# Performance work log

Measured on AMD Instinct MI355X. Metric: run time of the kernel, lower is better.

Reference implementation:

```python
import jax, jax.numpy as jnp
import numpy as np

B, N, IN_FEAT, HID, NHEAD, NLAYER, K = 8, 2048, 512, 128, 4, 3, 8
GRAPH_DIM = 32
EPS = 1e-5


def _layernorm(x, g, b):
    m = x.mean(-1, keepdims=True)
    v = ((x - m) ** 2).mean(-1, keepdims=True)
    return (x - m) * jax.lax.rsqrt(v + EPS) * g + b


def _knn_adj(cent):
    # cent [B,Ni,2] -> symmetric bool adjacency [B,Ni,Ni]; each node's k nearest
    # neighbours (self included, dist 0), then bidirected union (to_bidirected).
    d2 = jnp.sum((cent[:, :, None, :] - cent[:, None, :, :]) ** 2, -1)
    _, idx = jax.lax.top_k(-d2, K)  # [B,Ni,K]
    Bc, Nc = cent.shape[0], cent.shape[1]
    mask = jnp.zeros((Bc, Nc, Nc), bool).at[
        jnp.arange(Bc)[:, None, None], jnp.arange(Nc)[None, :, None], idx].set(True)
    return mask | jnp.swapaxes(mask, 1, 2)


def setup_inputs():
    key = jax.random.key(0)
    ks = jax.random.split(key, 12)
    s = 0.05
    H = HID
    return dict(
        feats=jax.random.normal(ks[0], (B, N, IN_FEAT), jnp.float32),
        cent=jax.random.uniform(ks[1], (B, N, 2), jnp.float32),
        Wp1=jax.random.normal(ks[2], (IN_FEAT, H)) * s, bp1=jnp.zeros((H,)),
        bn_g=jnp.ones((H,)), bn_b=jnp.zeros((H,)),
        Wp2=jax.random.normal(ks[3], (H, H)) * s, bp2=jnp.zeros((H,)),
        g1=jnp.ones((NLAYER, H)), be1=jnp.zeros((NLAYER, H)),
        g2=jnp.ones((NLAYER, H)), be2=jnp.zeros((NLAYER, H)),
        Ws=jax.random.normal(ks[4], (NLAYER, NHEAD, H, H)) * s,
        Wn=jax.random.normal(ks[5], (NLAYER, NHEAD, H, H)) * s,
        bs=jnp.zeros((NLAYER, NHEAD, H)),
        Wg=jax.random.normal(ks[6], (NLAYER, NHEAD * H, H)) * s,
        bg=jnp.zeros((NLAYER, H)),
        W1=jax.random.normal(ks[7], (NLAYER, H, H)) * s, b1=jnp.zeros((NLAYER, H)),
        W2=jax.random.normal(ks[8], (NLAYER, H, H)) * s, b2=jnp.zeros((NLAYER, H)),
        Wq=jax.random.normal(ks[9], (NLAYER, H, 1)) * s, bq=jnp.zeros((NLAYER,)),
        Wf1=jax.random.normal(ks[10], (2 * H, H)) * s, bf1=jnp.zeros((H,)),
        Wf2=jax.random.normal(ks[11], (H, GRAPH_DIM)) * s, bf2=jnp.zeros((GRAPH_DIM,)),
    )


def reference(feats, cent, Wp1, bp1, bn_g, bn_b, Wp2, bp2,
              g1, be1, g2, be2, Ws, Wn, bs, Wg, bg,
              W1, b1, W2, b2, Wq, bq, Wf1, bf1, Wf2, bf2):
    # preconv: Linear -> BatchNorm1d(eval: running mean 0 / var 1) -> ReLU -> Linear
    x = feats @ Wp1 + bp1
    x = x * (bn_g / jnp.sqrt(1.0 + EPS)) + bn_b
    x = jax.nn.relu(x) @ Wp2 + bp2              # [B,N,H]
    c = cent
    picks = 0.0
    for i in range(NLAYER):
        A = _knn_adj(c).astype(x.dtype)          # dynamic KNN graph, [B,Ni,Ni]
        deg = A.sum(-1)                          # in-degree (>=1, self loop)
        # GraphTransformerLayer: pre-LN -> multi-head mean SAGEConv -> residual
        xn = _layernorm(x, g1[i], be1[i])
        m = jnp.einsum('bij,bjd->bid', A, xn) / deg[..., None]
        h = jnp.einsum('bnd,hde->bnhe', xn, Ws[i]) \
            + jnp.einsum('bnd,hde->bnhe', m, Wn[i]) + bs[i]
        Bc, Nc = h.shape[0], h.shape[1]
        h = h.reshape(Bc, Nc, NHEAD * HID)       # concat heads on feature dim
        x = x + jax.nn.relu(h) @ Wg[i] + bg[i]
        # FFN block with residual
        xn2 = _layernorm(x, g2[i], be2[i])
        x = x + jax.nn.relu(xn2 @ W1[i] + b1[i]) @ W2[i] + b2[i]
        # SAGPool: GraphConv (symmetric norm) score -> top-k ratio 0.5 -> gate
        dinv = jax.lax.rsqrt(deg)
        s = dinv * jnp.einsum('bij,bj->bi', A, dinv * (x @ Wq[i])[..., 0]) + bq[i]
        kkeep = Nc // 2
        topv, topi = jax.lax.top_k(s, kkeep)     # per-graph top nodes
        x = jnp.take_along_axis(x, topi[..., None], axis=1) * jnp.tanh(topv)[..., None]
        c = jnp.take_along_axis(c, topi[..., None], axis=1)
        # max + avg readout on pooled graph
        picks = picks + jnp.concatenate([x.max(axis=1), x.mean(axis=1)], axis=-1)
    f = jax.nn.relu(picks @ Wf1 + bf1)
    f = jax.nn.relu(f @ Wf2 + bf2)               # [B, GRAPH_DIM]
    return f
```

## Files before the change

### kernel.cpp

```cpp
#include <hip/hip_runtime.h>
#include <math.h>

#define EPSV 1e-5f
#define GF_RELU 1
#define GF_ACCUM 2

typedef unsigned long long u64;
typedef unsigned int u32;
typedef unsigned short u16;
typedef float v2f __attribute__((ext_vector_type(2)));
typedef short bf16x8 __attribute__((ext_vector_type(8)));
typedef float f32x4 __attribute__((ext_vector_type(4)));

static const int Bn = 8;
static const int Nmax = 2048;
static const int KNN_K = 8;

__device__ __forceinline__ u32 split_pack(float v) {
  u32 u = __float_as_uint(v);
  float r = v - __uint_as_float(u & 0xffff0000u);
  return (u >> 16) | (__float_as_uint(r) & 0xffff0000u);
}

__device__ __forceinline__ void split4(float4 v, uint2& hp, uint2& lp) {
// ... 182 lines not shown
                                                        const float* __restrict__ be,
                                                        float* __restrict__ xn) {
  int row = blockIdx.x * 4 + (threadIdx.x >> 6);
  int lane = threadIdx.x & 63;
  const float* xr = x + (size_t)row * 128;
  float v1 = xr[lane], v2 = xr[lane + 64];
  float s = v1 + v2;
  for (int off = 32; off >= 1; off >>= 1) s += __shfl_xor(s, off, 64);
  float mean = s / 128.0f;
  float d1 = v1 - mean, d2 = v2 - mean;
  float q = d1 * d1 + d2 * d2;
  for (int off = 32; off >= 1; off >>= 1) q += __shfl_xor(q, off, 64);
  float rs = rsqrtf(q / 128.0f + EPSV);
  float* xo = xn + (size_t)row * 128;
  xo[lane] = d1 * rs * g[lane] + be[lane];
  xo[lane + 64] = d2 * rs * g[lane + 64] + be[lane + 64];
}

__global__ __launch_bounds__(256) void aggregate_kernel(const u32* __restrict__ adj,
                                                        const float* __restrict__ xn,
                                                        float* __restrict__ m,
                                                        float* __restrict__ dinv, int Ni) {
  int sub = threadIdx.x >> 7;
  int t = threadIdx.x & 127;
  int i = blockIdx.x * 2 + sub, b = blockIdx.y;
  __shared__ int cnt[2];
  extern __shared__ int list[];
  int* lst = list + sub * Ni;
  if (t == 0) cnt[sub] = 0;
  __syncthreads();
  int wpr = Ni >> 5;
  for (int w = t; w < wpr; w += 128) {
    u32 bits = adj[((size_t)(b * Nmax + i)) * 64 + w];
    while (bits) {
      int bit = __ffs(bits) - 1;
      bits &= bits - 1;
      int pos = atomicAdd(&cnt[sub], 1);
      lst[pos] = (w << 5) + bit;
    }
  }
  __syncthreads();
  int d = cnt[sub];
  float a0 = 0.0f, a1 = 0.0f;
  int k = 0;
  for (; k + 2 <= d; k += 2) {
    a0 += xn[((size_t)b * Ni + lst[k]) * 128 + t];
    a1 += xn[((size_t)b * Ni + lst[k + 1]) * 128 + t];
  }
  if (k < d) a0 += xn[((size_t)b * Ni + lst[k]) * 128 + t];
  m[((size_t)b * Ni + i) * 128 + t] = (a0 + a1) / (float)d;
  if (t == 0) dinv[b * Nmax + i] = 1.0f / sqrtf((float)d);
}

__global__ __launch_bounds__(256) void attn_gemm1_kernel(
    const float* __restrict__ XN, const float* __restrict__ MM,
    const u32* __restrict__ Wc, const float* __restrict__ bs,
    u16* __restrict__ Hh, u16* __restrict__ Hl, int M) {
  __shared__ u16 Ah[128][40], Al[128][40], Bh[128][40], Bl[128][40];
  int tid = threadIdx.x;
  int lane = tid & 63, w = tid >> 6;
  int wr = w >> 1, wc = w & 1;
  int lr = lane & 15, lk = (lane >> 4) * 8;
  int rowBase = blockIdx.y * 128, colBase = blockIdx.x * 128;
  f32x4 acc[4][4] = {};
  int arow = tid >> 1, aq = (tid & 1) * 16;
  int bcol = tid >> 1, bq = (tid & 1) * 16;

  float4 af[4];
  uint4 bf[4];
  {
    const float* Ap = XN + (size_t)(rowBase + arow) * 128 + aq;
#pragma unroll
    for (int q = 0; q < 4; ++q) af[q] = *(const float4*)(Ap + 4 * q);
    const u32* Bp = Wc + (size_t)(colBase + bcol) * 256 + bq;
#pragma unroll
    for (int q = 0; q < 4; ++q) bf[q] = *(const uint4*)(Bp + 4 * q);
  }
  for (int t = 0; t < 8; ++t) {
    __syncthreads();
#pragma unroll
    for (int q = 0; q < 4; ++q) {
      uint2 hp, lp;
      split4(af[q], hp, lp);
      *(uint2*)&Ah[arow][aq + 4 * q] = hp;
      *(uint2*)&Al[arow][aq + 4 * q] = lp;
      depair4(bf[q], hp, lp);
      *(uint2*)&Bh[bcol][bq + 4 * q] = hp;
      *(uint2*)&Bl[bcol][bq + 4 * q] = lp;
    }
    __syncthreads();
    if (t + 1 < 8) {
      const float* Asrc = (t + 1 < 4) ? XN : MM;
      int k0 = ((t + 1) & 3) * 32;
      const float* Ap = Asrc + (size_t)(rowBase + arow) * 128 + k0 + aq;
#pragma unroll
      for (int q = 0; q < 4; ++q) af[q] = *(const float4*)(Ap + 4 * q);
      const u32* Bp = Wc + (size_t)(colBase + bcol) * 256 + (t + 1) * 32 + bq;
#pragma unroll
      for (int q = 0; q < 4; ++q) bf[q] = *(const uint4*)(Bp + 4 * q);
    }
    bf16x8 ah[4], al[4], bh[4], bl[4];
#pragma unroll
    for (int mi = 0; mi < 4; ++mi) {
      int ar = wr * 64 + mi * 16 + lr;
      ah[mi] = *(const bf16x8*)&Ah[ar][lk];
      al[mi] = *(const bf16x8*)&Al[ar][lk];
    }
#pragma unroll
    for (int ni = 0; ni < 4; ++ni) {
      int bc = wc * 64 + ni * 16 + lr;
      bh[ni] = *(const bf16x8*)&Bh[bc][lk];
      bl[ni] = *(const bf16x8*)&Bl[bc][lk];
    }
#pragma unroll
    for (int mi = 0; mi < 4; ++mi)
#pragma unroll
      for (int ni = 0; ni < 4; ++ni) {
        f32x4 c = acc[mi][ni];
        c = __builtin_amdgcn_mfma_f32_16x16x32_bf16(al[mi], bh[ni], c, 0, 0, 0);
        c = __builtin_amdgcn_mfma_f32_16x16x32_bf16(ah[mi], bl[ni], c, 0, 0, 0);
        c = __builtin_amdgcn_mfma_f32_16x16x32_bf16(ah[mi], bh[ni], c, 0, 0, 0);
        acc[mi][ni] = c;
      }
  }
  int rq = (lane >> 4) * 4;
#pragma unroll
  for (int ni = 0; ni < 4; ++ni) {
    int col = colBase + wc * 64 + ni * 16 + lr;
    float bv = bs[col];
    size_t cbase = (size_t)(col >> 3) * 128 + (col & 7);
#pragma unroll
    for (int mi = 0; mi < 4; ++mi) {
      int rb = (rowBase >> 4) + wr * 4 + mi;
#pragma unroll
      for (int r = 0; r < 4; ++r) {
        float v = fmaxf(acc[mi][ni][r] + bv, 0.0f);
        u32 pr = split_pack(v);
        size_t o = (size_t)rb * 8192 + cbase + (size_t)(rq + r) * 8;
        Hh[o] = (u16)pr;
        Hl[o] = (u16)(pr >> 16);
      }
    }
  }
}

__global__ __launch_bounds__(256) void attn2_ffn16_kernel(
    const u16* __restrict__ Hh, const u16* __restrict__ Hl,
    const u16* __restrict__ Bgh, const u16* __restrict__ Bgl,
    const float* __restrict__ bg, const float* __restrict__ g,
    const float* __restrict__ be,
    const u16* __restrict__ W1h, const u16* __restrict__ W1l,
    const float* __restrict__ b1,
    const u16* __restrict__ W2h, const u16* __restrict__ W2l,
    const float* __restrict__ b2, float* __restrict__ x, int M) {
  __shared__ float XF[16][132];
  __shared__ u16 XH[16][136], XL[16][136];
  int tid = threadIdx.x;
  int lane = tid & 63, w = tid >> 6;
  int lr = lane & 15, lk = (lane >> 4) * 8, rq = (lane >> 4) * 4;
  int rowBase = blockIdx.x * 16;
  int colW = w * 32;
  int fo = (lane >> 4) * 128 + lr * 8;

  f32x4 acc[2] = {};
  {
    const u16* pAh = Hh + (size_t)blockIdx.x * 8192;
    const u16* pAl = Hl + (size_t)blockIdx.x * 8192;
    const u16* pBh = Bgh + (size_t)(w * 2) * 8192;
    const u16* pBl = Bgl + (size_t)(w * 2) * 8192;
    bf16x8 ah = *(const bf16x8*)(pAh + fo);
    bf16x8 al = *(const bf16x8*)(pAl + fo);
    bf16x8 b0h = *(const bf16x8*)(pBh + fo);
    bf16x8 b0l = *(const bf16x8*)(pBl + fo);
    bf16x8 b1h = *(const bf16x8*)(pBh + 8192 + fo);
    bf16x8 b1l = *(const bf16x8*)(pBl + 8192 + fo);
    for (int kt = 0; kt < 16; ++kt) {
      bf16x8 cah = ah, cal = al, cb0h = b0h, cb0l = b0l, cb1h = b1h, cb1l = b1l;
      if (kt + 1 < 16) {
        int off = (kt + 1) * 512 + fo;
        ah = *(const bf16x8*)(pAh + off);
        al = *(const bf16x8*)(pAl + off);
        b0h = *(const bf16x8*)(pBh + off);
        b0l = *(const bf16x8*)(pBl + off);
        b1h = *(const bf16x8*)(pBh + 8192 + off);
        b1l = *(const bf16x8*)(pBl + 8192 + off);
      }
      acc[0] = __builtin_amdgcn_mfma_f32_16x16x32_bf16(cal, cb0h, acc[0], 0, 0, 0);
      acc[0] = __builtin_amdgcn_mfma_f32_16x16x32_bf16(cah, cb0l, acc[0], 0, 0, 0);
      acc[0] = __builtin_amdgcn_mfma_f32_16x16x32_bf16(cah, cb0h, acc[0], 0, 0, 0);
      acc[1] = __builtin_amdgcn_mfma_f32_16x16x32_bf16(cal, cb1h, acc[1], 0, 0, 0);
      acc[1] = __builtin_amdgcn_mfma_f32_16x16x32_bf16(cah, cb1l, acc[1], 0, 0, 0);
      acc[1] = __builtin_amdgcn_mfma_f32_16x16x32_bf16(cah, cb1h, acc[1], 0, 0, 0);
    }
  }
#pragma unroll
  for (int ni = 0; ni < 2; ++ni) {
    int col = colW + ni * 16 + lr;
    float bv = bg[col];
#pragma unroll
    for (int r = 0; r < 4; ++r) {
      int rowL = rq + r;
      size_t o = (size_t)(rowBase + rowL) * 128 + col;
      float v = x[o] + acc[ni][r] + bv;
      x[o] = v;
      XF[rowL][col] = v;
    }
  }
  __syncthreads();
#pragma unroll
  for (int rr = 0; rr < 4; ++rr) {
    int rowL = w * 4 + rr;
    float v1 = XF[rowL][lane], v2 = XF[rowL][64 + lane];
    float s = v1 + v2;
    for (int off = 32; off >= 1; off >>= 1) s += __shfl_xor(s, off, 64);
    float mean = s / 128.0f;
    float d1 = v1 - mean, d2 = v2 - mean;
    float q = d1 * d1 + d2 * d2;
    for (int off = 32; off >= 1; off >>= 1) q += __shfl_xor(q, off, 64);
    float rs = rsqrtf(q / 128.0f + EPSV);
    float xn1 = d1 * rs * g[lane] + be[lane];
    float xn2 = d2 * rs * g[lane + 64] + be[lane + 64];
    u32 p1 = split_pack(xn1);
    u32 p2 = split_pack(xn2);
    XH[rowL][lane] = (u16)p1;  XL[rowL][lane] = (u16)(p1 >> 16);
    XH[rowL][64 + lane] = (u16)p2;  XL[rowL][64 + lane] = (u16)(p2 >> 16);
  }
  __syncthreads();
  f32x4 acc1[2] = {};
  {
    const u16* pBh = W1h + (size_t)(w * 2) * 2048;
    const u16* pBl = W1l + (size_t)(w * 2) * 2048;
#pragma unroll
    for (int kt = 0; kt < 4; ++kt) {
      int k0 = kt * 32 + lk;
      int off = kt * 512 + fo;
      bf16x8 ah = *(const bf16x8*)&XH[lr][k0];
      bf16x8 al = *(const bf16x8*)&XL[lr][k0];
      bf16x8 b0h = *(const bf16x8*)(pBh + off);
      bf16x8 b0l = *(const bf16x8*)(pBl + off);
      bf16x8 b1h = *(const bf16x8*)(pBh + 2048 + off);
      bf16x8 b1l = *(const bf16x8*)(pBl + 2048 + off);
      acc1[0] = __builtin_amdgcn_mfma_f32_16x16x32_bf16(al, b0h, acc1[0], 0, 0, 0);
      acc1[0] = __builtin_amdgcn_mfma_f32_16x16x32_bf16(ah, b0l, acc1[0], 0, 0, 0);
      acc1[0] = __builtin_amdgcn_mfma_f32_16x16x32_bf16(ah, b0h, acc1[0], 0, 0, 0);
      acc1[1] = __builtin_amdgcn_mfma_f32_16x16x32_bf16(al, b1h, acc1[1], 0, 0, 0);
      acc1[1] = __builtin_amdgcn_mfma_f32_16x16x32_bf16(ah, b1l, acc1[1], 0, 0, 0);
      acc1[1] = __builtin_amdgcn_mfma_f32_16x16x32_bf16(ah, b1h, acc1[1], 0, 0, 0);
    }
  }
  __syncthreads();
#pragma unroll
  for (int ni = 0; ni < 2; ++ni) {
    int col = colW + ni * 16 + lr;
    float bv = b1[col];
#pragma unroll
    for (int r = 0; r < 4; ++r) {
      int rowL = rq + r;
      float v = fmaxf(acc1[ni][r] + bv, 0.0f);
      u32 pr = split_pack(v);
      XH[rowL][col] = (u16)pr;
      XL[rowL][col] = (u16)(pr >> 16);
    }
  }
  __syncthreads();
  f32x4 acc2[2] = {};
  {
    const u16* pBh = W2h + (size_t)(w * 2) * 2048;
    const u16* pBl = W2l + (size_t)(w * 2) * 2048;
#pragma unroll
    for (int kt = 0; kt < 4; ++kt) {
      int k0 = kt * 32 + lk;
      int off = kt * 512 + fo;
      bf16x8 ah = *(const bf16x8*)&XH[lr][k0];
      bf16x8 al = *(const bf16x8*)&XL[lr][k0];
      bf16x8 b0h = *(const bf16x8*)(pBh + off);
      bf16x8 b0l = *(const bf16x8*)(pBl + off);
      bf16x8 b1h = *(const bf16x8*)(pBh + 2048 + off);
      bf16x8 b1l = *(const bf16x8*)(pBl + 2048 + off);
      acc2[0] = __builtin_amdgcn_mfma_f32_16x16x32_bf16(al, b0h, acc2[0], 0, 0, 0);
      acc2[0] = __builtin_amdgcn_mfma_f32_16x16x32_bf16(ah, b0l, acc2[0], 0, 0, 0);
      acc2[0] = __builtin_amdgcn_mfma_f32_16x16x32_bf16(ah, b0h, acc2[0], 0, 0, 0);
      acc2[1] = __builtin_amdgcn_mfma_f32_16x16x32_bf16(al, b1h, acc2[1], 0, 0, 0);
      acc2[1] = __builtin_amdgcn_mfma_f32_16x16x32_bf16(ah, b1l, acc2[1], 0, 0, 0);
      acc2[1] = __builtin_amdgcn_mfma_f32_16x16x32_bf16(ah, b1h, acc2[1], 0, 0, 0);
    }
  }
#pragma unroll
  for (int ni = 0; ni < 2; ++ni) {
    int col = colW + ni * 16 + lr;
    float bv = b2[col];
#pragma unroll
    for (int r = 0; r < 4; ++r) {
      int rowL = rq + r;
      size_t o = (size_t)(rowBase + rowL) * 128 + col;
      x[o] += acc2[ni][r] + bv;
    }
  }
}

__global__ __launch_bounds__(256) void preconv1_kernel(
    const float* __restrict__ F, const u32* __restrict__ WT,
    const float* __restrict__ sc, const float* __restrict__ bb,
    u32* __restrict__ H, int M) {
  __shared__ u16 Ah[64][40], Al[64][40], Bh[128][40], Bl[128][40];
  int tid = threadIdx.x;
  int lane = tid & 63, w = tid >> 6;
  int wr = w >> 1, wc = w & 1;
  int lr = lane & 15, lk = (lane >> 4) * 8;
  int rowBase = blockIdx.x * 64;
  f32x4 acc[2][4] = {};
  int arow = tid >> 2, aq = (tid & 3) * 8;
  int bcol = tid >> 1, bq = (tid & 1) * 16;

  float4 af[2];
  uint4 bf[4];
  {
    const float* Ap = F + (size_t)(rowBase + arow) * 512 + aq;
    af[0] = *(const float4*)Ap;
    af[1] = *(const float4*)(Ap + 4);
    const u32* Bp = WT + (size_t)bcol * 512 + bq;
#pragma unroll
    for (int q = 0; q < 4; ++q) bf[q] = *(const uint4*)(Bp + 4 * q);
  }
  for (int t = 0; t < 16; ++t) {
    __syncthreads();
    {
      uint2 hp, lp;
      split4(af[0], hp, lp);
      *(uint2*)&Ah[arow][aq] = hp; *(uint2*)&Al[arow][aq] = lp;
      split4(af[1], hp, lp);
      *(uint2*)&Ah[arow][aq + 4] = hp; *(uint2*)&Al[arow][aq + 4] = lp;
#pragma unroll
      for (int q = 0; q < 4; ++q) {
        depair4(bf[q], hp, lp);
        *(uint2*)&Bh[bcol][bq + 4 * q] = hp;
        *(uint2*)&Bl[bcol][bq + 4 * q] = lp;
      }
    }
    __syncthreads();
    if (t + 1 < 16) {
      int k0 = (t + 1) * 32;
      const float* Ap = F + (size_t)(rowBase + arow) * 512 + k0 + aq;
      af[0] = *(const float4*)Ap;
      af[1] = *(const float4*)(Ap + 4);
      const u32* Bp = WT + (size_t)bcol * 512 + k0 + bq;
#pragma unroll
      for (int q = 0; q < 4; ++q) bf[q] = *(const uint4*)(Bp + 4 * q);
    }
    bf16x8 ah[2], al[2], bh[4], bl[4];
#pragma unroll
    for (int mi = 0; mi < 2; ++mi) {
      int ar = wr * 32 + mi * 16 + lr;
      ah[mi] = *(const bf16x8*)&Ah[ar][lk];
      al[mi] = *(const bf16x8*)&Al[ar][lk];
    }
#pragma unroll
    for (int ni = 0; ni < 4; ++ni) {
      int bc = wc * 64 + ni * 16 + lr;
      bh[ni] = *(const bf16x8*)&Bh[bc][lk];
      bl[ni] = *(const bf16x8*)&Bl[bc][lk];
    }
#pragma unroll
    for (int mi = 0; mi < 2; ++mi)
#pragma unroll
      for (int ni = 0; ni < 4; ++ni) {
        f32x4 c = acc[mi][ni];
        c = __builtin_amdgcn_mfma_f32_16x16x32_bf16(al[mi], bh[ni], c, 0, 0, 0);
        c = __builtin_amdgcn_mfma_f32_16x16x32_bf16(ah[mi], bl[ni], c, 0, 0, 0);
        c = __builtin_amdgcn_mfma_f32_16x16x32_bf16(ah[mi], bh[ni], c, 0, 0, 0);
        acc[mi][ni] = c;
      }
  }
  int rq = (lane >> 4) * 4;
#pragma unroll
  for (int ni = 0; ni < 4; ++ni) {
    int col = wc * 64 + ni * 16 + lr;
    float s = sc[col], b = bb[col];
#pragma unroll
    for (int mi = 0; mi < 2; ++mi)
#pragma unroll
      for (int r = 0; r < 4; ++r) {
        int row = rowBase + wr * 32 + mi * 16 + rq + r;
        float v = fmaxf(acc[mi][ni][r] * s + b, 0.0f);
        H[(size_t)row * 128 + col] = split_pack(v);
      }
  }
}

__global__ __launch_bounds__(256) void preconv2_ln_kernel(
    const u32* __restrict__ H, const u32* __restrict__ WT,
    const float* __restrict__ bias, const float* __restrict__ g,
    const float* __restrict__ be, float* __restrict__ X,
    float* __restrict__ xn, int M) {
  __shared__ __align__(16) char smem[33792];
  u16* Ah = (u16*)smem;
  u16* Al = Ah + 64 * 40;
  u16* Bh = Al + 64 * 40;
  u16* Bl = Bh + 128 * 40;
  float* T = (float*)smem;
  int tid = threadIdx.x;
  int lane = tid & 63, w = tid >> 6;
  int wr = w >> 1, wc = w & 1;
  int lr = lane & 15, lk = (lane >> 4) * 8;
  int rowBase = blockIdx.x * 64;
  f32x4 acc[2][4] = {};
  int arow = tid >> 2, aq = (tid & 3) * 8;
  int bcol = tid >> 1, bq = (tid & 1) * 16;

  for (int kt = 0; kt < 4; ++kt) {
    __syncthreads();
    {
      const u32* Ap = H + (size_t)(rowBase + arow) * 128 + kt * 32 + aq;
      uint4 a0 = *(const uint4*)Ap, a1 = *(const uint4*)(Ap + 4);
      uint2 hp, lp;
      depair4(a0, hp, lp);
      *(uint2*)&Ah[arow * 40 + aq] = hp; *(uint2*)&Al[arow * 40 + aq] = lp;
      depair4(a1, hp, lp);
      *(uint2*)&Ah[arow * 40 + aq + 4] = hp; *(uint2*)&Al[arow * 40 + aq + 4] = lp;
      const u32* Bp = WT + (size_t)bcol * 128 + kt * 32 + bq;
#pragma unroll
      for (int q = 0; q < 4; ++q) {
        depair4(*(const uint4*)(Bp + 4 * q), hp, lp);
        *(uint2*)&Bh[bcol * 40 + bq + 4 * q] = hp;
        *(uint2*)&Bl[bcol * 40 + bq + 4 * q] = lp;
      }
    }
    __syncthreads();
    bf16x8 ah[2], al[2], bh[4], bl[4];
#pragma unroll
    for (int mi = 0; mi < 2; ++mi) {
      int ar = wr * 32 + mi * 16 + lr;
      ah[mi] = *(const bf16x8*)&Ah[ar * 40 + lk];
      al[mi] = *(const bf16x8*)&Al[ar * 40 + lk];
    }
#pragma unroll
    for (int ni = 0; ni < 4; ++ni) {
      int bc = wc * 64 + ni * 16 + lr;
      bh[ni] = *(const bf16x8*)&Bh[bc * 40 + lk];
      bl[ni] = *(const bf16x8*)&Bl[bc * 40 + lk];
    }
#pragma unroll
    for (int mi = 0; mi < 2; ++mi)
#pragma unroll
      for (int ni = 0; ni < 4; ++ni) {
        f32x4 c = acc[mi][ni];
        c = __builtin_amdgcn_mfma_f32_16x16x32_bf16(al[mi], bh[ni], c, 0, 0, 0);
        c = __builtin_amdgcn_mfma_f32_16x16x32_bf16(ah[mi], bl[ni], c, 0, 0, 0);
        c = __builtin_amdgcn_mfma_f32_16x16x32_bf16(ah[mi], bh[ni], c, 0, 0, 0);
        acc[mi][ni] = c;
// ... 509 lines not shown
        vp[c] = t;
      }
      size_t o = (size_t)row * N + col;
      if (flags & GF_ACCUM) {
        float4 old = *(float4*)&C[o];
        v.x += old.x; v.y += old.y; v.z += old.z; v.w += old.w;
      }
      *(float4*)&C[o] = v;
    }
  }
}

__global__ __launch_bounds__(256) void ffn_fused_kernel(
    const float* __restrict__ xn, const float* __restrict__ W1,
    const float* __restrict__ b1, const float* __restrict__ W2,
    const float* __restrict__ b2, float* __restrict__ x) {
  __shared__ float Axn[128 * 36];
  __shared__ float Hs [128 * 36];
  __shared__ float Bs [16 * 132];
  int tid = threadIdx.x;
  int rowBase = blockIdx.x * 32;
  int tx = tid & 31, ty = tid >> 5;
  {
    int row = tid >> 3, ks = (tid & 7) * 16;
    const float* s1 = xn + (size_t)(rowBase + row) * 128 + ks;
#pragma unroll
    for (int q = 0; q < 4; ++q) {
      float4 v = *(const float4*)(s1 + q * 4);
      int k = ks + q * 4;
      Axn[(k + 0) * 36 + row] = v.x; Axn[(k + 1) * 36 + row] = v.y;
      Axn[(k + 2) * 36 + row] = v.z; Axn[(k + 3) * 36 + row] = v.w;
    }
  }
  int bk = tid >> 4, bc = (tid & 15) * 8;
  v2f hacc[4][2] = {};
  {
    float4 p0 = *(const float4*)(W1 + (size_t)bk * 128 + bc);
    float4 p1 = *(const float4*)(W1 + (size_t)bk * 128 + bc + 4);
    for (int kt = 0; kt < 8; ++kt) {
      __syncthreads();
      *(float4*)&Bs[bk * 132 + bc] = p0;
      *(float4*)&Bs[bk * 132 + bc + 4] = p1;
      __syncthreads();
      if (kt < 7) {
        p0 = *(const float4*)(W1 + (size_t)(kt * 16 + 16 + bk) * 128 + bc);
        p1 = *(const float4*)(W1 + (size_t)(kt * 16 + 16 + bk) * 128 + bc + 4);
      }
      int k0 = kt * 16;
#pragma unroll
      for (int kk = 0; kk < 16; ++kk) {
        float av[4];
        v2f bv[2];
        *(float4*)av = *(const float4*)&Axn[(k0 + kk) * 36 + ty * 4];
        *(float4*)&bv[0] = *(const float4*)&Bs[kk * 132 + tx * 4];
#pragma unroll
        for (int r = 0; r < 4; ++r)
#pragma unroll
          for (int c = 0; c < 2; ++c) hacc[r][c] += av[r] * bv[c];
      }
    }
  }
  __syncthreads();
#pragma unroll
  for (int r = 0; r < 4; ++r) {
    float hv[4];
    *(v2f*)&hv[0] = hacc[r][0];
    *(v2f*)&hv[2] = hacc[r][1];
#pragma unroll
    for (int c = 0; c < 4; ++c) {
      float v = hv[c] + b1[tx * 4 + c];
      v = fmaxf(v, 0.0f);
      Hs[(tx * 4 + c) * 36 + ty * 4 + r] = v;
    }
  }
  v2f oacc[4][2] = {};
  {
    float4 q0 = *(const float4*)(W2 + (size_t)bk * 128 + bc);
    float4 q1 = *(const float4*)(W2 + (size_t)bk * 128 + bc + 4);
    for (int kt = 0; kt < 8; ++kt) {
      __syncthreads();
      *(float4*)&Bs[bk * 132 + bc] = q0;
      *(float4*)&Bs[bk * 132 + bc + 4] = q1;
      __syncthreads();
      if (kt < 7) {
        q0 = *(const float4*)(W2 + (size_t)(kt * 16 + 16 + bk) * 128 + bc);
        q1 = *(const float4*)(W2 + (size_t)(kt * 16 + 16 + bk) * 128 + bc + 4);
      }
      int k0 = kt * 16;
#pragma unroll
      for (int kk = 0; kk < 16; ++kk) {
        float av[4];
        v2f bv[2];
        *(float4*)av = *(const float4*)&Hs[(k0 + kk) * 36 + ty * 4];
        *(float4*)&bv[0] = *(const float4*)&Bs[kk * 132 + tx * 4];
#pragma unroll
        for (int r = 0; r < 4; ++r)
#pragma unroll
          for (int c = 0; c < 2; ++c) oacc[r][c] += av[r] * bv[c];
      }
    }
  }
#pragma unroll
  for (int r = 0; r < 4; ++r) {
    int row = rowBase + ty * 4 + r;
    float ov[4];
    *(v2f*)&ov[0] = oacc[r][0];
    *(v2f*)&ov[2] = oacc[r][1];
    float4 old = *(float4*)&x[(size_t)row * 128 + tx * 4];
    float4 v;
    v.x = ov[0] + b2[tx * 4 + 0]; v.x += old.x;
    v.y = ov[1] + b2[tx * 4 + 1]; v.y += old.y;
    v.z = ov[2] + b2[tx * 4 + 2]; v.z += old.z;
    v.w = ov[3] + b2[tx * 4 + 3]; v.w += old.w;
    *(float4*)&x[(size_t)row * 128 + tx * 4] = v;
  }
}

__global__ __launch_bounds__(256) void qp_kernel(const float* __restrict__ x,
                                                 const float* __restrict__ Wq,
                                                 const float* __restrict__ dinv,
                                                 float* __restrict__ p, int Ni) {
  int node = blockIdx.x * 4 + (threadIdx.x >> 6);
  int lane = threadIdx.x & 63;
  int b = node / Ni, i = node % Ni;
  float v = x[(size_t)node * 128 + lane] * Wq[lane] +
            x[(size_t)node * 128 + 64 + lane] * Wq[64 + lane];
  for (int off = 32; off >= 1; off >>= 1) v += __shfl_xor(v, off, 64);
  if (lane == 0) p[b * Nmax + i] = dinv[b * Nmax + i] * v;
}

__global__ __launch_bounds__(256) void score_kernel(const u32* __restrict__ adj,
                                                    const float* __restrict__ p,
                                                    const float* __restrict__ dinv,
                                                    const float* __restrict__ bq,
                                                    float* __restrict__ s, int Ni) {
  int i = blockIdx.x * 4 + (threadIdx.x >> 6);
  int b = blockIdx.y, lane = threadIdx.x & 63;
  int wpr = Ni >> 5;
  float acc = 0.0f;
  if (lane < wpr) {
    u32 bits = adj[((size_t)(b * Nmax + i)) * 64 + lane];
    while (bits) {
      int bit = __ffs(bits) - 1;
      bits &= bits - 1;
      acc += p[b * Nmax + (lane << 5) + bit];
    }
  }
  for (int off = 32; off >= 1; off >>= 1) acc += __shfl_xor(acc, off, 64);
  if (lane == 0) s[b * Nmax + i] = dinv[b * Nmax + i] * acc + bq[0];
}

__global__ void topk_rank_kernel(const float* __restrict__ s, int Ni, int* __restrict__ topi) {
  int b = blockIdx.y;
  int e0 = blockIdx.x * 256;
  int t = threadIdx.x;
  __shared__ u64 keys[2048];
  for (int e = t; e < Ni; e += 256) {
    u32 u = __float_as_uint(s[b * Nmax + e]);
    u32 mono = (u & 0x80000000u) ? ~u : (u | 0x80000000u);
    keys[e] = ((u64)(~mono) << 32) | (u32)e;
  }
  __syncthreads();
  int e = e0 + t;
  if (e >= Ni) return;
  u64 my = keys[e];
  int rank = 0;
  for (int q = 0; q < Ni; q += 4) {
    rank += (keys[q] < my) ? 1 : 0;
    rank += (keys[q + 1] < my) ? 1 : 0;
    rank += (keys[q + 2] < my) ? 1 : 0;
    rank += (keys[q + 3] < my) ? 1 : 0;
  }
  int kkeep = Ni >> 1;
  if (rank < kkeep) topi[b * 1024 + rank] = e;
}

__global__ __launch_bounds__(256) void gather_kernel(
    const float* __restrict__ x, const float* __restrict__ c,
    const float* __restrict__ s, const int* __restrict__ topi,
    float* __restrict__ xo, float* __restrict__ co,
    const float* __restrict__ g, const float* __restrict__ be,
    float* __restrict__ xn, int Ni) {
  int inew = blockIdx.x * 4 + (threadIdx.x >> 6);
  int b = blockIdx.y, lane = threadIdx.x & 63;
  int kkeep = Ni >> 1;
  int old = topi[b * 1024 + inew];
  float gate = tanhf(s[b * Nmax + old]);
  size_t ri = ((size_t)b * Ni + old) * 128;
  size_t ro = ((size_t)b * kkeep + inew) * 128;
  float v1 = x[ri + lane] * gate;
  float v2 = x[ri + 64 + lane] * gate;
  xo[ro + lane] = v1;
  xo[ro + 64 + lane] = v2;
  if (lane < 2) co[((size_t)b * kkeep + inew) * 2 + lane] = c[((size_t)b * Ni + old) * 2 + lane];
  if (g) {
    float sm = v1 + v2;
    for (int off = 32; off >= 1; off >>= 1) sm += __shfl_xor(sm, off, 64);
    float mean = sm / 128.0f;
    float d1 = v1 - mean, d2 = v2 - mean;
    float q = d1 * d1 + d2 * d2;
    for (int off = 32; off >= 1; off >>= 1) q += __shfl_xor(q, off, 64);
    float rs = rsqrtf(q / 128.0f + EPSV);
    xn[ro + lane] = d1 * rs * g[lane] + be[lane];
    xn[ro + 64 + lane] = d2 * rs * g[lane + 64] + be[lane + 64];
  }
}

__global__ void picks_partial_kernel(const float* __restrict__ x, float* __restrict__ part,
                                     int kkeep, int G) {
  int b = blockIdx.x, g = blockIdx.y, t = threadIdx.x;
  int per = kkeep / G;
  int start = g * per;
  float mx = -INFINITY, sm = 0.0f;
  for (int i = start; i < start + per; ++i) {
    float v = x[((size_t)b * kkeep + i) * 128 + t];
    mx = fmaxf(mx, v);
    sm += v;
  }
  part[((size_t)(b * G + g)) * 256 + t] = mx;
  part[((size_t)(b * G + g)) * 256 + 128 + t] = sm;
}

__global__ void picks_combine_kernel(const float* __restrict__ part, float* __restrict__ picks,
                                     int kkeep, int G) {
  int b = blockIdx.x, t = threadIdx.x;
  float mx = -INFINITY, sm = 0.0f;
  for (int g = 0; g < G; ++g) {
    mx = fmaxf(mx, part[((size_t)(b * G + g)) * 256 + t]);
    sm += part[((size_t)(b * G + g)) * 256 + 128 + t];
  }
  picks[b * 256 + t] += mx;
  picks[b * 256 + 128 + t] += sm / (float)kkeep;
}

__global__ void final_kernel(const float* __restrict__ picks, const float* __restrict__ Wf1,
                             const float* __restrict__ bf1, const float* __restrict__ Wf2,
                             const float* __restrict__ bf2, float* __restrict__ out) {
  int b = blockIdx.x, t = threadIdx.x;
  __shared__ float pk[256];
  __shared__ float fm[128];
  pk[t] = picks[b * 256 + t];
  pk[t + 128] = picks[b * 256 + 128 + t];
  __syncthreads();
  float acc = bf1[t];
  for (int k = 0; k < 256; ++k) acc += pk[k] * Wf1[k * 128 + t];
  fm[t] = fmaxf(acc, 0.0f);
  __syncthreads();
  if (t < 32) {
    float a2 = bf2[t];
    for (int k = 0; k < 128; ++k) a2 += fm[k] * Wf2[k * 32 + t];
    out[b * 32 + t] = fmaxf(a2, 0.0f);
  }
}

extern "C" void kernel_launch(void* const* d_in, const int* in_sizes, int n_in,
                              void* d_out, int out_size, void* d_ws, size_t ws_size,
                              hipStream_t stream) {
  const float* feats = (const float*)d_in[0];
  const float* cent  = (const float*)d_in[1];
  const float* Wp1 = (const float*)d_in[2];
  const float* bp1 = (const float*)d_in[3];
  const float* bn_g = (const float*)d_in[4];
  const float* bn_b = (const float*)d_in[5];
  const float* Wp2 = (const float*)d_in[6];
  const float* bp2 = (const float*)d_in[7];
  const float* g1  = (const float*)d_in[8];
  const float* be1 = (const float*)d_in[9];
  const float* g2  = (const float*)d_in[10];
  const float* be2 = (const float*)d_in[11];
  const float* Ws  = (const float*)d_in[12];
  const float* Wn  = (const float*)d_in[13];
  const float* bs  = (const float*)d_in[14];
  const float* Wg  = (const float*)d_in[15];
  const float* bg  = (const float*)d_in[16];
  const float* W1  = (const float*)d_in[17];
  const float* b1  = (const float*)d_in[18];
  const float* W2  = (const float*)d_in[19];
  const float* b2  = (const float*)d_in[20];
  const float* Wq  = (const float*)d_in[21];
  const float* bq  = (const float*)d_in[22];
  const float* Wf1 = (const float*)d_in[23];
  const float* bf1 = (const float*)d_in[24];
  const float* Wf2 = (const float*)d_in[25];
  const float* bf2 = (const float*)d_in[26];
  float* out = (float*)d_out;

  float* p = (float*)d_ws;
  const size_t SZX = (size_t)Bn * Nmax * 128;
  float* SC = p;    p += 128;
  float* BBv = p;   p += 128;
  float* DINV = p;  p += Bn * Nmax;
  float* PV = p;    p += Bn * Nmax;
  float* SS = p;    p += Bn * Nmax;
  float* PICKS = p; p += Bn * 256;
  float* PART = p;  p += (size_t)Bn * 32 * 256;
  float* C0 = p;    p += (size_t)Bn * Nmax * 2;
  float* C1 = p;    p += (size_t)Bn * Nmax * 2;
  int* KNN = (int*)p;  p += (size_t)Bn * Nmax * KNN_K;
  int* TOPI = (int*)p; p += Bn * 1024;
  u32* ADJ = (u32*)p;  p += (size_t)Bn * Nmax * 64;
  float* X0 = p;    p += SZX;
  float* X1 = p;    p += SZX;
  float* BA = p;    p += SZX;
  float* BB = p;    p += SZX;
  float* HB = p;
  size_t base_floats = (size_t)(p - (float*)d_ws);
  const size_t WPSZ = (size_t)3 * 128 * 512;
  bool fused = ws_size >= (base_floats + 4 * SZX + 2 * WPSZ) * sizeof(float);
  float* WSP = HB + 4 * SZX;
  float* WNP = WSP + WPSZ;
  float* PK = WNP + WPSZ;
  bool fused2 = ws_size >= (base_floats + 8 * SZX + 2 * WPSZ) * sizeof(float);
  bool fused3 = ws_size >= (base_floats + 9 * SZX + 2 * WPSZ) * sizeof(float);

  u16* WgTh = (u16*)PK;
  u16* WgTl = WgTh + 196608;
  u32* Wp1Tu = (u32*)PK + 196608;
  u32* Wp2Tu = Wp1Tu + 65536;
  u32* W1Tu  = Wp2Tu + 16384;
  u16* W1Th = (u16*)W1Tu;
  u16* W1Tl = W1Th + 49152;
  u32* W2Tu  = W1Tu + 49152;
  u16* W2Th = (u16*)W2Tu;
  u16* W2Tl = W2Th + 49152;
  u16* Hh = (u16*)HB;
  u16* Hl = Hh + (size_t)Bn * Nmax * 512;

  hipLaunchKernelGGL(precompute_kernel, dim3(1), dim3(256), 0, stream,
                     bn_g, bn_b, bp1, SC, BBv, PICKS);
  if (fused3) {
    hipLaunchKernelGGL(repack_split_kernel, dim3(3008), dim3(256), 0, stream,
                       Ws, Wn, Wg, Wp1, Wp2, W1, W2,
                       (u32*)WSP, WgTh, WgTl, Wp1Tu, Wp2Tu, W1Th, W1Tl, W2Th, W2Tl);
  } else if (fused) {
    hipLaunchKernelGGL(repack_ws_kernel, dim3(768), dim3(256), 0, stream, Ws, Wn, WSP, WNP);
  }

  const int M0 = Bn * Nmax;
  if (fused3) {
    hipLaunchKernelGGL(preconv1_kernel, dim3(M0 / 64), dim3(256), 0, stream,
                       feats, Wp1Tu, SC, BBv, (u32*)HB, M0);
    hipLaunchKernelGGL(preconv2_ln_kernel, dim3(M0 / 64), dim3(256), 0, stream,
                       (const u32*)HB, Wp2Tu, bp2, g1, be1, X0, BA, M0);
  } else if (fused) {
    hipLaunchKernelGGL(gemm128ks_kernel, dim3(1, M0 / 128, 4), dim3(256), 0, stream,
                       feats, Wp1, HB, M0, 512);
    hipLaunchKernelGGL(gemm_psum4_kernel, dim3(1, M0 / 32), dim3(256), 0, stream,
                       HB, SC, BBv, Wp2, bp2, X0, M0);
  } else {
    hipLaunchKernelGGL(gemm_kernel<32>, dim3(1, M0 / 32), dim3(256), 0, stream,
                       feats, Wp1, (const float*)nullptr, (const float*)nullptr,
                       SC, BBv, BA, M0, 128, 512, GF_RELU);
    hipLaunchKernelGGL(gemm_kernel<32>, dim3(1, M0 / 32), dim3(256), 0, stream,
                       BA, Wp2, (const float*)nullptr, (const float*)nullptr,
                       (const float*)nullptr, bp2, X0, M0, 128, 128, 0);
  }

  float* xc = X0;
  float* xo = X1;
  const float* cc = cent;
  float* co = C0;
  int Ni = Nmax;
  for (int L = 0; L < 3; ++L) {
    int M = Bn * Ni;
    if (Ni == 2048)      hipLaunchKernelGGL(knn_sel_kernel<32>, dim3(Ni / 4, Bn), dim3(256), 0, stream, cc, KNN, Ni);
    else if (Ni == 1024) hipLaunchKernelGGL(knn_sel_kernel<16>, dim3(Ni / 4, Bn), dim3(256), 0, stream, cc, KNN, Ni);
    else                 hipLaunchKernelGGL(knn_sel_kernel<8>,  dim3(Ni / 4, Bn), dim3(256), 0, stream, cc, KNN, Ni);
    hipMemsetAsync(ADJ, 0, (size_t)Bn * Nmax * 64 * sizeof(u32), stream);
    int tot = Bn * Ni * KNN_K;
    hipLaunchKernelGGL(build_adj_kernel, dim3((tot + 255) / 256), dim3(256), 0, stream,
                       KNN, ADJ, Ni);
    if (!fused3) {
      hipLaunchKernelGGL(layernorm_kernel, dim3(M / 4), dim3(256), 0, stream,
                         xc, g1 + L * 128, be1 + L * 128, BA);
    }
    hipLaunchKernelGGL(aggregate_kernel, dim3(Ni / 2, Bn), dim3(256), 2 * Ni * sizeof(int), stream,
                       ADJ, BA, BB, DINV, Ni);
    if (fused3) {
      hipLaunchKernelGGL(attn_gemm1_kernel, dim3(4, M / 128), dim3(256), 0, stream,
                         BA, BB, (const u32*)WSP + (size_t)L * 512 * 256,
                         bs + L * 512, Hh, Hl, M);
      hipLaunchKernelGGL(attn2_ffn16_kernel, dim3(M / 16), dim3(256), 0, stream,
                         Hh, Hl,
                         WgTh + (size_t)L * 65536, WgTl + (size_t)L * 65536,
                         bg + L * 128, g2 + L * 128, be2 + L * 128,
                         W1Th + (size_t)L * 16384, W1Tl + (size_t)L * 16384,
                         b1 + L * 128,
                         W2Th + (size_t)L * 16384, W2Tl + (size_t)L * 16384,
                         b2 + L * 128, xc, M);
    } else if (fused2) {
      hipLaunchKernelGGL(gemm128dual_kernel, dim3(4, M / 128, 2), dim3(256), 0, stream,
                         BA, WSP + (size_t)L * 128 * 512,
                         BB, WNP + (size_t)L * 128 * 512,
                         HB, PK, M, 512);
      hipLaunchKernelGGL(gemm_hsum_kernel, dim3(1, M / 32), dim3(256), 0, stream,
                         HB, PK, bs + L * 512, Wg + (size_t)L * 512 * 128,
                         bg + L * 128, xc, M);
      hipLaunchKernelGGL(layernorm_kernel, dim3(M / 4), dim3(256), 0, stream,
                         xc, g2 + L * 128, be2 + L * 128, BA);
      hipLaunchKernelGGL(ffn_fused_kernel, dim3(M / 32), dim3(256), 0, stream,
                         BA, W1 + (size_t)L * 128 * 128, b1 + L * 128,
                         W2 + (size_t)L * 128 * 128, b2 + L * 128, xc);
    } else if (fused) {
      hipLaunchKernelGGL(gemm128_kernel, dim3(4, M / 128), dim3(256), 0, stream,
                         BA, WSP + (size_t)L * 128 * 512,
                         BB, WNP + (size_t)L * 128 * 512,
                         bs + L * 512, HB, M, 512, 128, GF_RELU);
      hipLaunchKernelGGL(gemm_kernel<32>, dim3(1, M / 32), dim3(256), 0, stream,
                         HB, Wg + (size_t)L * 512 * 128,
                         (const float*)nullptr, (const float*)nullptr,
                         (const float*)nullptr, bg + L * 128,
                         xc, M, 128, 512, GF_ACCUM);
      hipLaunchKernelGGL(layernorm_kernel, dim3(M / 4), dim3(256), 0, stream,
                         xc, g2 + L * 128, be2 + L * 128, BA);
      hipLaunchKernelGGL(ffn_fused_kernel, dim3(M / 32), dim3(256), 0, stream,
                         BA, W1 + (size_t)L * 128 * 128, b1 + L * 128,
                         W2 + (size_t)L * 128 * 128, b2 + L * 128, xc);
    } else {
      for (int hh = 0; hh < 4; ++hh) {
        hipLaunchKernelGGL(gemm_kernel<32>, dim3(1, M / 32), dim3(256), 0, stream,
                           BA, Ws + ((size_t)(L * 4 + hh)) * 128 * 128,
                           BB, Wn + ((size_t)(L * 4 + hh)) * 128 * 128,
                           (const float*)nullptr, bs + (L * 4 + hh) * 128,
                           HB, M, 128, 128, GF_RELU);
        hipLaunchKernelGGL(gemm_kernel<32>, dim3(1, M / 32), dim3(256), 0, stream,
                           HB, Wg + ((size_t)L * 512 + hh * 128) * 128,
                           (const float*)nullptr, (const float*)nullptr,
                           (const float*)nullptr, (hh == 0) ? (bg + L * 128) : (const float*)nullptr,
                           xc, M, 128, 128, GF_ACCUM);
      }
      hipLaunchKernelGGL(layernorm_kernel, dim3(M / 4), dim3(256), 0, stream,
                         xc, g2 + L * 128, be2 + L * 128, BA);
      hipLaunchKernelGGL(ffn_fused_kernel, dim3(M / 32), dim3(256), 0, stream,
                         BA, W1 + (size_t)L * 128 * 128, b1 + L * 128,
                         W2 + (size_t)L * 128 * 128, b2 + L * 128, xc);
    }
    hipLaunchKernelGGL(qp_kernel, dim3(M / 4), dim3(256), 0, stream, xc, Wq + L * 128, DINV, PV, Ni);
    hipLaunchKernelGGL(score_kernel, dim3(Ni / 4, Bn), dim3(256), 0, stream, ADJ, PV, DINV, bq + L, SS, Ni);
    hipLaunchKernelGGL(topk_rank_kernel, dim3((Ni + 255) / 256, Bn), dim3(256), 0, stream,
                       SS, Ni, TOPI);
    int kkeep = Ni >> 1;
    const float* gn = (fused3 && L < 2) ? (g1 + (L + 1) * 128) : (const float*)nullptr;
    const float* bn = (fused3 && L < 2) ? (be1 + (L + 1) * 128) : (const float*)nullptr;
    hipLaunchKernelGGL(gather_kernel, dim3(kkeep / 4, Bn), dim3(256), 0, stream,
                       xc, cc, SS, TOPI, xo, co, gn, bn, BA, Ni);
    int G = kkeep / 32;
    hipLaunchKernelGGL(picks_partial_kernel, dim3(Bn, G), dim3(128), 0, stream,
                       xo, PART, kkeep, G);
    hipLaunchKernelGGL(picks_combine_kernel, dim3(Bn), dim3(128), 0, stream,
                       PART, PICKS, kkeep, G);
    float* tmp = xc; xc = xo; xo = tmp;
    cc = co;
    co = (co == C0) ? C1 : C0;
    Ni = kkeep;
  }
  hipLaunchKernelGGL(final_kernel, dim3(Bn), dim3(128), 0, stream,
                     PICKS, Wf1, bf1, Wf2, bf2, out);
}
```

Measured before the change: 524.2 us.

## Fuse Wq projection into FFN, gather with pick partials, split top-k ranking

The FFN epilogue now computes the per-node Wq dot product through shuffle and shared-memory atomic reductions and writes dinv-scaled PV directly, so the separate qp kernel is skipped on the fused path. The gather kernel now also produces the max/sum readout partials, which removes the picks_partial launch and a reread of the pooled features. The top-k rank kernel splits each element's comparison loop across four waves and sums the partial ranks, giving more blocks and a shorter serial loop. Together these cut launches and memory traffic, at the cost of extra shared-memory atomics and syncs in the FFN kernel.

Result: faster. 494.9 us (-5.6%).

```diff
diff --git a/kernel.cpp b/kernel.cpp
--- a/kernel.cpp
+++ b/kernel.cpp
@@ -358,9 +358,12 @@
     const u16* __restrict__ W1h, const u16* __restrict__ W1l,
     const float* __restrict__ b1,
     const u16* __restrict__ W2h, const u16* __restrict__ W2l,
-    const float* __restrict__ b2, float* __restrict__ x, int M) {
+    const float* __restrict__ b2, float* __restrict__ x,
+    const float* __restrict__ Wq, const float* __restrict__ dinv,
+    float* __restrict__ PV, int niShift, int M) {
   __shared__ float XF[16][132];
   __shared__ u16 XH[16][136], XL[16][136];
+  __shared__ float QS[16];
   int tid = threadIdx.x;
   int lane = tid & 63, w = tid >> 6;
   int lr = lane & 15, lk = (lane >> 4) * 8, rq = (lane >> 4) * 4;
@@ -455,6 +458,7 @@
     }
   }
   __syncthreads();
+  if (tid < 16) QS[tid] = 0.0f;
 #pragma unroll
   for (int ni = 0; ni < 2; ++ni) {
     int col = colW + ni * 16 + lr;
@@ -491,16 +495,38 @@
       acc2[1] = __builtin_amdgcn_mfma_f32_16x16x32_bf16(ah, b1h, acc2[1], 0, 0, 0);
     }
   }
+  float qp[4] = {0.0f, 0.0f, 0.0f, 0.0f};
 #pragma unroll
   for (int ni = 0; ni < 2; ++ni) {
     int col = colW + ni * 16 + lr;
     float bv = b2[col];
+    float wq = Wq[col];
 #pragma unroll
     for (int r = 0; r < 4; ++r) {
       int rowL = rq + r;
       size_t o = (size_t)(rowBase + rowL) * 128 + col;
-      x[o] += acc2[ni][r] + bv;
-    }
+      float v = x[o] + acc2[ni][r] + bv;
+      x[o] = v;
+      qp[r] += v * wq;
+    }
+  }
+#pragma unroll
+  for (int r = 0; r < 4; ++r) {
+    qp[r] += __shfl_xor(qp[r], 1, 64);
+    qp[r] += __shfl_xor(qp[r], 2, 64);
+    qp[r] += __shfl_xor(qp[r], 4, 64);
+    qp[r] += __shfl_xor(qp[r], 8, 64);
+  }
+  if (lr == 0) {
+#pragma unroll
+    for (int r = 0; r < 4; ++r) atomicAdd(&QS[rq + r], qp[r]);
+  }
+  __syncthreads();
+  if (tid < 16) {
+    int node = rowBase + tid;
+    int bb = node >> niShift;
+    int ii = node & ((1 << niShift) - 1);
+    PV[bb * Nmax + ii] = dinv[bb * Nmax + ii] * QS[tid];
   }
 }
 
@@ -1316,73 +1342,83 @@
 
 __global__ void topk_rank_kernel(const float* __restrict__ s, int Ni, int* __restrict__ topi) {
   int b = blockIdx.y;
-  int e0 = blockIdx.x * 256;
+  int e0 = blockIdx.x * 64;
   int t = threadIdx.x;
   __shared__ u64 keys[2048];
+  __shared__ int PR[256];
   for (int e = t; e < Ni; e += 256) {
     u32 u = __float_as_uint(s[b * Nmax + e]);
     u32 mono = (u & 0x80000000u) ? ~u : (u | 0x80000000u);
     keys[e] = ((u64)(~mono) << 32) | (u32)e;
   }
   __syncthreads();
-  int e = e0 + t;
-  if (e >= Ni) return;
-  u64 my = keys[e];
+  int quad = t >> 6, eloc = t & 63;
+  u64 my = keys[e0 + eloc];
+  int seg = Ni >> 2;
+  int s0 = quad * seg;
   int rank = 0;
-  for (int q = 0; q < Ni; q += 4) {
-    rank += (keys[q] < my) ? 1 : 0;
-    rank += (keys[q + 1] < my) ? 1 : 0;
-    rank += (keys[q + 2] < my) ? 1 : 0;
-    rank += (keys[q + 3] < my) ? 1 : 0;
-  }
-  int kkeep = Ni >> 1;
-  if (rank < kkeep) topi[b * 1024 + rank] = e;
-}
-
-__global__ __launch_bounds__(256) void gather_kernel(
+  for (int k = s0; k < s0 + seg; k += 4) {
+    rank += (keys[k] < my) ? 1 : 0;
+    rank += (keys[k + 1] < my) ? 1 : 0;
+    rank += (keys[k + 2] < my) ? 1 : 0;
+    rank += (keys[k + 3] < my) ? 1 : 0;
+  }
+  PR[t] = rank;
+  __syncthreads();
+  if (t < 64) {
+    int tot = PR[t] + PR[t + 64] + PR[t + 128] + PR[t + 192];
+    int kkeep = Ni >> 1;
+    if (tot < kkeep) topi[b * 1024 + tot] = e0 + t;
+  }
+}
+
+__global__ __launch_bounds__(256) void gather_pick_kernel(
     const float* __restrict__ x, const float* __restrict__ c,
     const float* __restrict__ s, const int* __restrict__ topi,
     float* __restrict__ xo, float* __restrict__ co,
     const float* __restrict__ g, const float* __restrict__ be,
-    float* __restrict__ xn, int Ni) {
-  int inew = blockIdx.x * 4 + (threadIdx.x >> 6);
-  int b = blockIdx.y, lane = threadIdx.x & 63;
+    float* __restrict__ xn, float* __restrict__ part, int Ni) {
+  int gblk = blockIdx.x, b = blockIdx.y;
+  int w = threadIdx.x >> 6, lane = threadIdx.x & 63;
   int kkeep = Ni >> 1;
-  int old = topi[b * 1024 + inew];
-  float gate = tanhf(s[b * Nmax + old]);
-  size_t ri = ((size_t)b * Ni + old) * 128;
-  size_t ro = ((size_t)b * kkeep + inew) * 128;
-  float v1 = x[ri + lane] * gate;
-  float v2 = x[ri + 64 + lane] * gate;
-  xo[ro + lane] = v1;
-  xo[ro + 64 + lane] = v2;
-  if (lane < 2) co[((size_t)b * kkeep + inew) * 2 + lane] = c[((size_t)b * Ni + old) * 2 + lane];
-  if (g) {
-    float sm = v1 + v2;
-    for (int off = 32; off >= 1; off >>= 1) sm += __shfl_xor(sm, off, 64);
-    float mean = sm / 128.0f;
-    float d1 = v1 - mean, d2 = v2 - mean;
-    float q = d1 * d1 + d2 * d2;
-    for (int off = 32; off >= 1; off >>= 1) q += __shfl_xor(q, off, 64);
-    float rs = rsqrtf(q / 128.0f + EPSV);
-    xn[ro + lane] = d1 * rs * g[lane] + be[lane];
-    xn[ro + 64 + lane] = d2 * rs * g[lane + 64] + be[lane + 64];
-  }
-}
-
-__global__ void picks_partial_kernel(const float* __restrict__ x, float* __restrict__ part,
-                                     int kkeep, int G) {
-  int b = blockIdx.x, g = blockIdx.y, t = threadIdx.x;
-  int per = kkeep / G;
-  int start = g * per;
-  float mx = -INFINITY, sm = 0.0f;
-  for (int i = start; i < start + per; ++i) {
-    float v = x[((size_t)b * kkeep + i) * 128 + t];
-    mx = fmaxf(mx, v);
-    sm += v;
-  }
-  part[((size_t)(b * G + g)) * 256 + t] = mx;
-  part[((size_t)(b * G + g)) * 256 + 128 + t] = sm;
+  float mx1 = -INFINITY, mx2 = -INFINITY, sm1 = 0.0f, sm2 = 0.0f;
+  for (int r2 = 0; r2 < 8; ++r2) {
+    int inew = gblk * 32 + w * 8 + r2;
+    int old = topi[b * 1024 + inew];
+    float gate = tanhf(s[b * Nmax + old]);
+    size_t ri = ((size_t)b * Ni + old) * 128;
+    size_t ro = ((size_t)b * kkeep + inew) * 128;
+    float v1 = x[ri + lane] * gate;
+    float v2 = x[ri + 64 + lane] * gate;
+    xo[ro + lane] = v1;
+    xo[ro + 64 + lane] = v2;
+    if (lane < 2) co[((size_t)b * kkeep + inew) * 2 + lane] = c[((size_t)b * Ni + old) * 2 + lane];
+    mx1 = fmaxf(mx1, v1); mx2 = fmaxf(mx2, v2);
+    sm1 += v1; sm2 += v2;
+    if (g) {
+      float sm = v1 + v2;
+      for (int off = 32; off >= 1; off >>= 1) sm += __shfl_xor(sm, off, 64);
+      float mean = sm / 128.0f;
+      float d1 = v1 - mean, d2 = v2 - mean;
+      float q = d1 * d1 + d2 * d2;
+      for (int off = 32; off >= 1; off >>= 1) q += __shfl_xor(q, off, 64);
+      float rs = rsqrtf(q / 128.0f + EPSV);
+      xn[ro + lane] = d1 * rs * g[lane] + be[lane];
+      xn[ro + 64 + lane] = d2 * rs * g[lane + 64] + be[lane + 64];
+    }
+  }
+  __shared__ float LM[4][128], LS[4][128];
+  LM[w][lane] = mx1; LM[w][64 + lane] = mx2;
+  LS[w][lane] = sm1; LS[w][64 + lane] = sm2;
+  __syncthreads();
+  int t = threadIdx.x;
+  if (t < 128) {
+    float m = fmaxf(fmaxf(LM[0][t], LM[1][t]), fmaxf(LM[2][t], LM[3][t]));
+    float ss = (LS[0][t] + LS[1][t]) + (LS[2][t] + LS[3][t]);
+    size_t base = ((size_t)(b * (kkeep >> 5) + gblk)) * 256;
+    part[base + t] = m;
+    part[base + 128 + t] = ss;
+  }
 }
 
 __global__ void picks_combine_kernel(const float* __restrict__ part, float* __restrict__ picks,
@@ -1527,6 +1563,7 @@
   int Ni = Nmax;
   for (int L = 0; L < 3; ++L) {
     int M = Bn * Ni;
+    int niShift = (Ni == 2048) ? 11 : (Ni == 1024) ? 10 : 9;
     if (Ni == 2048)      hipLaunchKernelGGL(knn_sel_kernel<32>, dim3(Ni / 4, Bn), dim3(256), 0, stream, cc, KNN, Ni);
     else if (Ni == 1024) hipLaunchKernelGGL(knn_sel_kernel<16>, dim3(Ni / 4, Bn), dim3(256), 0, stream, cc, KNN, Ni);
     else                 hipLaunchKernelGGL(knn_sel_kernel<8>,  dim3(Ni / 4, Bn), dim3(256), 0, stream, cc, KNN, Ni);
@@ -1551,7 +1588,8 @@
                          W1Th + (size_t)L * 16384, W1Tl + (size_t)L * 16384,
                          b1 + L * 128,
                          W2Th + (size_t)L * 16384, W2Tl + (size_t)L * 16384,
-                         b2 + L * 128, xc, M);
+                         b2 + L * 128, xc,
+                         Wq + L * 128, DINV, PV, niShift, M);
     } else if (fused2) {
       hipLaunchKernelGGL(gemm128dual_kernel, dim3(4, M / 128, 2), dim3(256), 0, stream,
                          BA, WSP + (size_t)L * 128 * 512,
@@ -1599,18 +1637,18 @@
                          BA, W1 + (size_t)L * 128 * 128, b1 + L * 128,
                          W2 + (size_t)L * 128 * 128, b2 + L * 128, xc);
     }
-    hipLaunchKernelGGL(qp_kernel, dim3(M / 4), dim3(256), 0, stream, xc, Wq + L * 128, DINV, PV, Ni);
+    if (!fused3) {
+      hipLaunchKernelGGL(qp_kernel, dim3(M / 4), dim3(256), 0, stream, xc, Wq + L * 128, DINV, PV, Ni);
+    }
     hipLaunchKernelGGL(score_kernel, dim3(Ni / 4, Bn), dim3(256), 0, stream, ADJ, PV, DINV, bq + L, SS, Ni);
-    hipLaunchKernelGGL(topk_rank_kernel, dim3((Ni + 255) / 256, Bn), dim3(256), 0, stream,
+    hipLaunchKernelGGL(topk_rank_kernel, dim3(Ni / 64, Bn), dim3(256), 0, stream,
                        SS, Ni, TOPI);
     int kkeep = Ni >> 1;
     const float* gn = (fused3 && L < 2) ? (g1 + (L + 1) * 128) : (const float*)nullptr;
     const float* bn = (fused3 && L < 2) ? (be1 + (L + 1) * 128) : (const float*)nullptr;
-    hipLaunchKernelGGL(gather_kernel, dim3(kkeep / 4, Bn), dim3(256), 0, stream,
-                       xc, cc, SS, TOPI, xo, co, gn, bn, BA, Ni);
+    hipLaunchKernelGGL(gather_pick_kernel, dim3(kkeep / 32, Bn), dim3(256), 0, stream,
+                       xc, cc, SS, TOPI, xo, co, gn, bn, BA, PART, Ni);
     int G = kkeep / 32;
-    hipLaunchKernelGGL(picks_partial_kernel, dim3(Bn, G), dim3(128), 0, stream,
-                       xo, PART, kkeep, G);
     hipLaunchKernelGGL(picks_combine_kernel, dim3(Bn), dim3(128), 0, stream,
                        PART, PICKS, kkeep, G);
     float* tmp = xc; xc = xo; xo = tmp;
```
